# Performance work log

Measured on AMD Instinct MI355X. Metric: run time of the kernel, lower is better.

Reference implementation:

```python
import jax, jax.numpy as jnp
import numpy as np

V, H, B = 64, 128, 16384  # num_visible, num_hidden = alpha*V, batch of spin configs
ISCALE = 0.001


def setup_inputs() -> dict:
    key = jax.random.key(0)
    k1, k2, k3, k4 = jax.random.split(key, 4)
    x = jax.random.normal(k1, (B, V), dtype=jnp.float32)
    weight_1 = jax.random.normal(k2, (V, H), dtype=jnp.float32) * ISCALE
    weight_2 = jax.random.normal(k3, (H, V, V), dtype=jnp.float32) * (ISCALE / 10.0)
    hidden_bias = jax.random.normal(k4, (H,), dtype=jnp.float32) * ISCALE
    return {"x": x, "weight_1": weight_1, "weight_2": weight_2, "hidden_bias": hidden_bias}


def reference(x, weight_1, weight_2, hidden_bias):
    b, v = x.shape
    h = weight_2.shape[0]
    # order-1 term: (B,V) @ (V,H) -> (B,H)
    w1 = x @ weight_1
    # order-2 term: outer product of spins per sample, contracted with weight_2.
    # vis_ij: (B,V,V) flattened to (B,V*V); weight_2 flattened to (H,V*V) -> GEMM.
    vis_ij = jnp.einsum('mi,mj->mij', x, x).reshape(b, v * v)
    w2 = (vis_ij @ weight_2.reshape(h, v * v).T) * 0.5
    act = jnp.cos(hidden_bias + w1 + w2)  # (B,H)
    psi = jnp.prod(act, axis=-1)          # (B,)
    return psi
```

## Files before the change

### kernel.cpp

```cpp
#include <hip/hip_runtime.h>
#include <hip/hip_bf16.h>
#include <cstdint>

#define NV 64
#define NH 128
#define NB 16384
#define NCHUNK 37
#define FRAG_ELEMS (NCHUNK * 8192)

typedef __bf16 bf16x8_t __attribute__((ext_vector_type(8)));
typedef float f32x4_t __attribute__((ext_vector_type(4)));
typedef float f32x2_t __attribute__((ext_vector_type(2)));
typedef uint32_t u32x4_t __attribute__((ext_vector_type(4)));
typedef uint32_t u32x2_t __attribute__((ext_vector_type(2)));

__device__ __forceinline__ uint32_t bf16_rne(float f) {
  uint32_t u = __float_as_uint(f);
  return (u + 0x7fffu + ((u >> 16) & 1u)) >> 16;
}

__global__ void cvt_kernel(const float* __restrict__ w1f,
                           const float* __restrict__ w2f,
                           uint16_t* __restrict__ frag) {
  int tg = blockIdx.x * 256 + threadIdx.x;
  int l = tg & 63, fh = (tg >> 6) & 7, c2 = tg >> 9;
  int chunk = c2 >> 1, jh = c2 & 1;
  int h = fh * 16 + (l & 15);
  int kb = jh * 32 + (l >> 4) * 8;
  uint32_t o16[8];
#pragma unroll
  for (int t = 0; t < 8; ++t) {
    int slot = kb + t;
    float v;
    if (chunk < 8) {
      int i = chunk * 8 + (slot >> 3), j = chunk * 8 + (slot & 7);
      v = 0.5f * w2f[h * 4096 + i * 64 + j];
    } else if (chunk < 36) {
      int o = chunk - 8, I = 0;
      while (o >= 7 - I) { o -= 7 - I; ++I; }
      int J = I + 1 + o;
      int i = I * 8 + (slot >> 3), j = J * 8 + (slot & 7);
      v = 0.5f * (w2f[h * 4096 + i * 64 + j] + w2f[h * 4096 + j * 64 + i]);
    } else {
      v = w1f[slot * 128 + h];
    }
    o16[t] = bf16_rne(v);
  }
  uint4 o;
  o.x = (o16[1] << 16) | o16[0];
  o.y = (o16[3] << 16) | o16[2];
  o.z = (o16[5] << 16) | o16[4];
  o.w = (o16[7] << 16) | o16[6];
  *(uint4*)(frag + ((size_t)(c2 * 8 + fh) << 9) + l * 8) = o;
}

__launch_bounds__(512, 2)
__global__ void rbm_kernel(const float* __restrict__ xg,
                           const float* __restrict__ biasg,
                           const __hip_bfloat16* __restrict__ frag,
                           float* __restrict__ outg) {
  __shared__ __align__(16) float xtile[64 * 76];
  __shared__ float part[4][64];

  const int tid  = threadIdx.x;
  const int wv   = tid >> 6;
  const int wm   = wv & 1;
  const int hq   = wv >> 1;
  const int lane = tid & 63;
  const int c15  = lane & 15;
  const int q    = lane >> 4;
  const int mblk = blockIdx.x * 64;

  constexpr int CI[36] = {0,1,2,3,4,5,6,7, 0,0,0,0,0,0,0, 1,1,1,1,1,1,
                          2,2,2,2,2, 3,3,3,3, 4,4,4, 5,5, 6};
  constexpr int CJ[36] = {0,1,2,3,4,5,6,7, 1,2,3,4,5,6,7, 2,3,4,5,6,7,
                          3,4,5,6,7, 4,5,6,7, 5,6,7, 6,7, 7};

  {
    int row = tid >> 3, grp = tid & 7;
    const float* p = xg + (size_t)(mblk + row) * NV + grp * 8;
    float4 a = *(const float4*)(p);
    float4 b = *(const float4*)(p + 4);
    *(float4*)(&xtile[row * 76 + grp * 8]) = a;
    *(float4*)(&xtile[row * 76 + grp * 8 + 4]) = b;
    xtile[row * 76 + 64 + grp] = 1.0f;
  }
  __syncthreads();

  const float* sx[2];
  f32x2_t xb[2][32];
#pragma unroll
  for (int im = 0; im < 2; ++im) {
    sx[im] = &xtile[(wm * 32 + im * 16 + c15) * 76];
#pragma unroll
    for (int g = 0; g < 8; ++g) {
      float4 a = *(const float4*)(sx[im] + g * 8);
      float4 b = *(const float4*)(sx[im] + g * 8 + 4);
      xb[im][g * 4 + 0] = f32x2_t{a.x, a.y};
      xb[im][g * 4 + 1] = f32x2_t{a.z, a.w};
      xb[im][g * 4 + 2] = f32x2_t{b.x, b.y};
      xb[im][g * 4 + 3] = f32x2_t{b.z, b.w};
    }
  }

  const __hip_bfloat16* pw = frag + (size_t)hq * 1024 + lane * 8;

  f32x4_t acc[2][2];
#pragma unroll
  for (int im = 0; im < 2; ++im)
#pragma unroll
    for (int ih = 0; ih < 2; ++ih)
      acc[im][ih] = (f32x4_t)0.0f;

  bf16x8_t bn[2][2];
#pragma unroll
  for (int jh = 0; jh < 2; ++jh)
#pragma unroll
    for (int ih = 0; ih < 2; ++ih)
      bn[jh][ih] = *(const bf16x8_t*)(pw + jh * 4096 + ih * 512);

#pragma unroll
  for (int c = 0; c < 36; ++c) {
    bf16x8_t bc[2][2];
#pragma unroll
    for (int jh = 0; jh < 2; ++jh)
#pragma unroll
      for (int ih = 0; ih < 2; ++ih)
        bc[jh][ih] = bn[jh][ih];
    {
      const __hip_bfloat16* pn = pw + (size_t)(c + 1) * 8192;
#pragma unroll
      for (int jh = 0; jh < 2; ++jh)
#pragma unroll
        for (int ih = 0; ih < 2; ++ih)
          bn[jh][ih] = *(const bf16x8_t*)(pn + jh * 4096 + ih * 512);
    }
    const int I = CI[c], J = CJ[c];
#pragma unroll
    for (int jh = 0; jh < 2; ++jh) {
      bf16x8_t afrag[2];
#pragma unroll
      for (int im = 0; im < 2; ++im) {
        float s = sx[im][I * 8 + jh * 4 + q];
        const f32x2_t s2 = f32x2_t{s, s};
        u32x4_t adv;
#pragma unroll
        for (int tt = 0; tt < 4; ++tt) {
          f32x2_t pr = s2 * xb[im][J * 4 + tt];
          u32x2_t u = __builtin_bit_cast(u32x2_t, pr);
          adv[tt] = __builtin_amdgcn_perm(u[1], u[0], 0x07060302);
        }
        afrag[im] = __builtin_bit_cast(bf16x8_t, adv);
      }
#pragma unroll
      for (int ih = 0; ih < 2; ++ih)
#pragma unroll
        for (int im = 0; im < 2; ++im)
          acc[im][ih] = __builtin_amdgcn_mfma_f32_16x16x32_bf16(
              afrag[im], bc[jh][ih], acc[im][ih], 0, 0, 0);
    }
  }

#pragma unroll
  for (int jh = 0; jh < 2; ++jh) {
    bf16x8_t afrag[2];
#pragma unroll
    for (int im = 0; im < 2; ++im) {
      float4 a = *(const float4*)(sx[im] + jh * 32 + q * 8);
      float4 b = *(const float4*)(sx[im] + jh * 32 + q * 8 + 4);
      const float pr[4][2] = {{a.x, a.y}, {a.z, a.w}, {b.x, b.y}, {b.z, b.w}};
      u32x4_t adv;
#pragma unroll
      for (int tt = 0; tt < 4; ++tt)
        adv[tt] = __builtin_amdgcn_perm(__float_as_uint(pr[tt][1]),
                                        __float_as_uint(pr[tt][0]), 0x07060302);
      afrag[im] = __builtin_bit_cast(bf16x8_t, adv);
    }
#pragma unroll
    for (int ih = 0; ih < 2; ++ih)
#pragma unroll
      for (int im = 0; im < 2; ++im)
        acc[im][ih] = __builtin_amdgcn_mfma_f32_16x16x32_bf16(
            afrag[im], bn[jh][ih], acc[im][ih], 0, 0, 0);
  }

  float bs[2];
#pragma unroll
  for (int ih = 0; ih < 2; ++ih)
    bs[ih] = biasg[hq * 32 + ih * 16 + c15];

  const float INV2PI = 0.15915494309189535f;
  float prod[2][4];
#pragma unroll
  for (int im = 0; im < 2; ++im)
#pragma unroll
    for (int r = 0; r < 4; ++r) {
      float c0 = __builtin_amdgcn_cosf((acc[im][0][r] + bs[0]) * INV2PI);
      float c1 = __builtin_amdgcn_cosf((acc[im][1][r] + bs[1]) * INV2PI);
      prod[im][r] = c0 * c1;
    }

#pragma unroll
  for (int ofs = 1; ofs < 16; ofs <<= 1)
#pragma unroll
    for (int im = 0; im < 2; ++im)
#pragma unroll
      for (int r = 0; r < 4; ++r)
        prod[im][r] *= __shfl_xor(prod[im][r], ofs, 16);

  if (c15 == 0) {
#pragma unroll
    for (int im = 0; im < 2; ++im)
#pragma unroll
      for (int r = 0; r < 4; ++r)
        part[hq][wm * 32 + im * 16 + q * 4 + r] = prod[im][r];
  }
  __syncthreads();
  if (tid < 64) {
    float f = part[0][tid] * part[1][tid] * part[2][tid] * part[3][tid];
    outg[mblk + tid] = f;
  }
}

extern "C" void kernel_launch(void* const* d_in, const int* in_sizes, int n_in,
                              void* d_out, int out_size, void* d_ws, size_t ws_size,
                              hipStream_t stream) {
  const float* x   = (const float*)d_in[0];
  const float* w1f = (const float*)d_in[1];
  const float* w2f = (const float*)d_in[2];
  const float* hb  = (const float*)d_in[3];
  float* out = (float*)d_out;
  uint16_t* frag = (uint16_t*)d_ws;
  (void)in_sizes; (void)n_in; (void)out_size; (void)ws_size;

  cvt_kernel<<<148, 256, 0, stream>>>(w1f, w2f, frag);
  rbm_kernel<<<NB / 64, 512, 0, stream>>>(
      x, hb, (const __hip_bfloat16*)frag, out);
}
```

Baseline: 86.38 us.

## Halve rows per block to cut registers and raise occupancy

Each block now processes 32 samples instead of 64, so each wave handles one 16-row M tile rather than two. This halves the per-thread x registers and accumulators and allows launch bounds of 4 blocks per CU, doubling the grid. The weight-fragment prefetch is also interleaved directly with the MFMAs instead of copying a double buffer. The cost is half the reuse of each loaded weight fragment, so global/L2 traffic for weights doubles.

Measured after the change: 87.13 us. Within noise of the previous version (+0.9%).

```diff
diff --git a/kernel.cpp b/kernel.cpp
--- a/kernel.cpp
+++ b/kernel.cpp
@@ -54,13 +54,13 @@
   *(uint4*)(frag + ((size_t)(c2 * 8 + fh) << 9) + l * 8) = o;
 }
 
-__launch_bounds__(512, 2)
+__launch_bounds__(512, 4)
 __global__ void rbm_kernel(const float* __restrict__ xg,
                            const float* __restrict__ biasg,
                            const __hip_bfloat16* __restrict__ frag,
                            float* __restrict__ outg) {
-  __shared__ __align__(16) float xtile[64 * 76];
-  __shared__ float part[4][64];
+  __shared__ __align__(16) float xtile[32 * 76];
+  __shared__ float part[4][32];
 
   const int tid  = threadIdx.x;
   const int wv   = tid >> 6;
@@ -69,7 +69,7 @@
   const int lane = tid & 63;
   const int c15  = lane & 15;
   const int q    = lane >> 4;
-  const int mblk = blockIdx.x * 64;
+  const int mblk = blockIdx.x * 32;
 
   constexpr int CI[36] = {0,1,2,3,4,5,6,7, 0,0,0,0,0,0,0, 1,1,1,1,1,1,
                           2,2,2,2,2, 3,3,3,3, 4,4,4, 5,5, 6};
@@ -77,111 +77,81 @@
                           3,4,5,6,7, 4,5,6,7, 5,6,7, 6,7, 7};
 
   {
-    int row = tid >> 3, grp = tid & 7;
-    const float* p = xg + (size_t)(mblk + row) * NV + grp * 8;
-    float4 a = *(const float4*)(p);
-    float4 b = *(const float4*)(p + 4);
-    *(float4*)(&xtile[row * 76 + grp * 8]) = a;
-    *(float4*)(&xtile[row * 76 + grp * 8 + 4]) = b;
-    xtile[row * 76 + 64 + grp] = 1.0f;
+    int row = tid >> 4, col4 = (tid & 15) * 4;
+    const float* p = xg + (size_t)(mblk + row) * NV + col4;
+    *(float4*)(&xtile[row * 76 + col4]) = *(const float4*)p;
   }
   __syncthreads();
 
-  const float* sx[2];
-  f32x2_t xb[2][32];
-#pragma unroll
-  for (int im = 0; im < 2; ++im) {
-    sx[im] = &xtile[(wm * 32 + im * 16 + c15) * 76];
-#pragma unroll
-    for (int g = 0; g < 8; ++g) {
-      float4 a = *(const float4*)(sx[im] + g * 8);
-      float4 b = *(const float4*)(sx[im] + g * 8 + 4);
-      xb[im][g * 4 + 0] = f32x2_t{a.x, a.y};
-      xb[im][g * 4 + 1] = f32x2_t{a.z, a.w};
-      xb[im][g * 4 + 2] = f32x2_t{b.x, b.y};
-      xb[im][g * 4 + 3] = f32x2_t{b.z, b.w};
+  const float* sx = &xtile[(wm * 16 + c15) * 76];
+  f32x2_t xb[32];
+#pragma unroll
+  for (int g = 0; g < 8; ++g) {
+    float4 a = *(const float4*)(sx + g * 8);
+    float4 b4 = *(const float4*)(sx + g * 8 + 4);
+    xb[g * 4 + 0] = f32x2_t{a.x, a.y};
+    xb[g * 4 + 1] = f32x2_t{a.z, a.w};
+    xb[g * 4 + 2] = f32x2_t{b4.x, b4.y};
+    xb[g * 4 + 3] = f32x2_t{b4.z, b4.w};
+  }
+
+  const __hip_bfloat16* pw = frag + (size_t)hq * 1024 + lane * 8;
+
+  f32x4_t acc[2];
+#pragma unroll
+  for (int ih = 0; ih < 2; ++ih)
+    acc[ih] = (f32x4_t)0.0f;
+
+  bf16x8_t b[4];
+#pragma unroll
+  for (int jh = 0; jh < 2; ++jh)
+#pragma unroll
+    for (int ih = 0; ih < 2; ++ih)
+      b[jh * 2 + ih] = *(const bf16x8_t*)(pw + jh * 4096 + ih * 512);
+
+#pragma unroll
+  for (int c = 0; c < 36; ++c) {
+    const int I = CI[c], J = CJ[c];
+    bf16x8_t afrag[2];
+#pragma unroll
+    for (int jh = 0; jh < 2; ++jh) {
+      float s = sx[I * 8 + jh * 4 + q];
+      const f32x2_t s2 = f32x2_t{s, s};
+      u32x4_t adv;
+#pragma unroll
+      for (int tt = 0; tt < 4; ++tt) {
+        f32x2_t pr = s2 * xb[J * 4 + tt];
+        u32x2_t u = __builtin_bit_cast(u32x2_t, pr);
+        adv[tt] = __builtin_amdgcn_perm(u[1], u[0], 0x07060302);
+      }
+      afrag[jh] = __builtin_bit_cast(bf16x8_t, adv);
     }
-  }
-
-  const __hip_bfloat16* pw = frag + (size_t)hq * 1024 + lane * 8;
-
-  f32x4_t acc[2][2];
-#pragma unroll
-  for (int im = 0; im < 2; ++im)
+    const __hip_bfloat16* pn = pw + (size_t)(c + 1) * 8192;
+#pragma unroll
+    for (int jh = 0; jh < 2; ++jh)
+#pragma unroll
+      for (int ih = 0; ih < 2; ++ih) {
+        acc[ih] = __builtin_amdgcn_mfma_f32_16x16x32_bf16(
+            afrag[jh], b[jh * 2 + ih], acc[ih], 0, 0, 0);
+        b[jh * 2 + ih] = *(const bf16x8_t*)(pn + jh * 4096 + ih * 512);
+      }
+  }
+
+#pragma unroll
+  for (int jh = 0; jh < 2; ++jh) {
+    float4 a = *(const float4*)(sx + jh * 32 + q * 8);
+    float4 b4 = *(const float4*)(sx + jh * 32 + q * 8 + 4);
+    const float pr[4][2] = {{a.x, a.y}, {a.z, a.w}, {b4.x, b4.y}, {b4.z, b4.w}};
+    u32x4_t adv;
+#pragma unroll
+    for (int tt = 0; tt < 4; ++tt)
+      adv[tt] = __builtin_amdgcn_perm(__float_as_uint(pr[tt][1]),
+                                      __float_as_uint(pr[tt][0]), 0x07060302);
+    bf16x8_t af = __builtin_bit_cast(bf16x8_t, adv);
 #pragma unroll
     for (int ih = 0; ih < 2; ++ih)
-      acc[im][ih] = (f32x4_t)0.0f;
-
-  bf16x8_t bn[2][2];
-#pragma unroll
-  for (int jh = 0; jh < 2; ++jh)
-#pragma unroll
-    for (int ih = 0; ih < 2; ++ih)
-      bn[jh][ih] = *(const bf16x8_t*)(pw + jh * 4096 + ih * 512);
-
-#pragma unroll
-  for (int c = 0; c < 36; ++c) {
-    bf16x8_t bc[2][2];
-#pragma unroll
-    for (int jh = 0; jh < 2; ++jh)
-#pragma unroll
-      for (int ih = 0; ih < 2; ++ih)
-        bc[jh][ih] = bn[jh][ih];
-    {
-      const __hip_bfloat16* pn = pw + (size_t)(c + 1) * 8192;
-#pragma unroll
-      for (int jh = 0; jh < 2; ++jh)
-#pragma unroll
-        for (int ih = 0; ih < 2; ++ih)
-          bn[jh][ih] = *(const bf16x8_t*)(pn + jh * 4096 + ih * 512);
-    }
-    const int I = CI[c], J = CJ[c];
-#pragma unroll
-    for (int jh = 0; jh < 2; ++jh) {
-      bf16x8_t afrag[2];
-#pragma unroll
-      for (int im = 0; im < 2; ++im) {
-        float s = sx[im][I * 8 + jh * 4 + q];
-        const f32x2_t s2 = f32x2_t{s, s};
-        u32x4_t adv;
-#pragma unroll
-        for (int tt = 0; tt < 4; ++tt) {
-          f32x2_t pr = s2 * xb[im][J * 4 + tt];
-          u32x2_t u = __builtin_bit_cast(u32x2_t, pr);
-          adv[tt] = __builtin_amdgcn_perm(u[1], u[0], 0x07060302);
-        }
-        afrag[im] = __builtin_bit_cast(bf16x8_t, adv);
-      }
-#pragma unroll
-      for (int ih = 0; ih < 2; ++ih)
-#pragma unroll
-        for (int im = 0; im < 2; ++im)
-          acc[im][ih] = __builtin_amdgcn_mfma_f32_16x16x32_bf16(
-              afrag[im], bc[jh][ih], acc[im][ih], 0, 0, 0);
-    }
-  }
-
-#pragma unroll
-  for (int jh = 0; jh < 2; ++jh) {
-    bf16x8_t afrag[2];
-#pragma unroll
-    for (int im = 0; im < 2; ++im) {
-      float4 a = *(const float4*)(sx[im] + jh * 32 + q * 8);
-      float4 b = *(const float4*)(sx[im] + jh * 32 + q * 8 + 4);
-      const float pr[4][2] = {{a.x, a.y}, {a.z, a.w}, {b.x, b.y}, {b.z, b.w}};
-      u32x4_t adv;
-#pragma unroll
-      for (int tt = 0; tt < 4; ++tt)
-        adv[tt] = __builtin_amdgcn_perm(__float_as_uint(pr[tt][1]),
-                                        __float_as_uint(pr[tt][0]), 0x07060302);
-      afrag[im] = __builtin_bit_cast(bf16x8_t, adv);
-    }
-#pragma unroll
-    for (int ih = 0; ih < 2; ++ih)
-#pragma unroll
-      for (int im = 0; im < 2; ++im)
-        acc[im][ih] = __builtin_amdgcn_mfma_f32_16x16x32_bf16(
-            afrag[im], bn[jh][ih], acc[im][ih], 0, 0, 0);
+      acc[ih] = __builtin_amdgcn_mfma_f32_16x16x32_bf16(
+          af, b[jh * 2 + ih], acc[ih], 0, 0, 0);
   }
 
   float bs[2];
@@ -190,33 +160,27 @@
     bs[ih] = biasg[hq * 32 + ih * 16 + c15];
 
   const float INV2PI = 0.15915494309189535f;
-  float prod[2][4];
-#pragma unroll
-  for (int im = 0; im < 2; ++im)
-#pragma unroll
-    for (int r = 0; r < 4; ++r) {
-      float c0 = __builtin_amdgcn_cosf((acc[im][0][r] + bs[0]) * INV2PI);
-      float c1 = __builtin_amdgcn_cosf((acc[im][1][r] + bs[1]) * INV2PI);
-      prod[im][r] = c0 * c1;
-    }
+  float prod[4];
+#pragma unroll
+  for (int r = 0; r < 4; ++r) {
+    float c0 = __builtin_amdgcn_cosf((acc[0][r] + bs[0]) * INV2PI);
+    float c1 = __builtin_amdgcn_cosf((acc[1][r] + bs[1]) * INV2PI);
+    prod[r] = c0 * c1;
+  }
 
 #pragma unroll
   for (int ofs = 1; ofs < 16; ofs <<= 1)
 #pragma unroll
-    for (int im = 0; im < 2; ++im)
-#pragma unroll
-      for (int r = 0; r < 4; ++r)
-        prod[im][r] *= __shfl_xor(prod[im][r], ofs, 16);
+    for (int r = 0; r < 4; ++r)
+      prod[r] *= __shfl_xor(prod[r], ofs, 16);
 
   if (c15 == 0) {
 #pragma unroll
-    for (int im = 0; im < 2; ++im)
-#pragma unroll
-      for (int r = 0; r < 4; ++r)
-        part[hq][wm * 32 + im * 16 + q * 4 + r] = prod[im][r];
+    for (int r = 0; r < 4; ++r)
+      part[hq][wm * 16 + q * 4 + r] = prod[r];
   }
   __syncthreads();
-  if (tid < 64) {
+  if (tid < 32) {
     float f = part[0][tid] * part[1][tid] * part[2][tid] * part[3][tid];
     outg[mblk + tid] = f;
   }
@@ -234,6 +198,6 @@
   (void)in_sizes; (void)n_in; (void)out_size; (void)ws_size;
 
   cvt_kernel<<<148, 256, 0, stream>>>(w1f, w2f, frag);
-  rbm_kernel<<<NB / 64, 512, 0, stream>>>(
+  rbm_kernel<<<NB / 32, 512, 0, stream>>>(
       x, hb, (const __hip_bfloat16*)frag, out);
 }
```
